# Kernel tuning notes

Hardware: AMD Instinct MI355X
Metric: run time of the kernel (lower is better)

## Reference

```python
import jax, jax.numpy as jnp
import numpy as np

NUM_EXPERTS = 16
CAPACITY = 1024  # expert_capacity


def setup_inputs() -> dict:
    key = jax.random.key(0)
    ks = jax.random.split(key, 5)
    B, D, H, O = 8192, 1024, 4096, 1024
    E = NUM_EXPERTS
    sc = lambda k, shp, fan: jax.random.normal(k, shp, jnp.float32) * (1.0 / np.sqrt(fan))
    return {
        "x": jax.random.normal(ks[0], (B, D), jnp.float32),
        "Wr": sc(ks[1], (D, E), D),
        "br": jnp.zeros((E,), jnp.float32),
        "W1": sc(ks[2], (E, D, H), D),
        "b1": jnp.zeros((E, H), jnp.float32),
        "W2": sc(ks[3], (E, H, O), H),
        "b2": jnp.zeros((E, O), jnp.float32),
    }


def reference(x, Wr, br, W1, b1, W2, b2):
    B = x.shape[0]
    E = Wr.shape[1]
    O = W2.shape[-1]
    cap = min(CAPACITY, B)

    router_logits = x @ Wr + br                 # [B, E]
    # NOTE: softmax over the TOKEN axis (dim=0), as in the source (expert-choice)
    router_probs = jax.nn.softmax(router_logits, axis=0)

    # each expert picks its top-`cap` tokens
    top_scores, top_idx = jax.lax.top_k(router_probs.T, cap)   # [E, cap]

    sel = x[top_idx]                            # [E, cap, D] gather
    h = jax.nn.relu(jnp.einsum('ecd,edh->ech', sel, W1) + b1[:, None, :])
    # dropout_prob=0 -> identity in eval/our config
    eo = jnp.einsum('ech,eho->eco', h, W2) + b2[:, None, :]    # [E, cap, O]

    contrib = eo * top_scores[..., None]        # weight by routing score
    output = jnp.zeros((B, O), x.dtype).at[top_idx.reshape(-1)].add(
        contrib.reshape(-1, O))                 # scatter-add combine

    expert_mask = jnp.zeros((B, E), x.dtype).at[
        top_idx, jnp.arange(E)[:, None]].set(1.0)
    return output, router_probs, expert_mask
```

## Files before the change

### kernel.cpp

```cpp
#include <hip/hip_runtime.h>

typedef unsigned short u16;
typedef unsigned int   u32;
typedef unsigned long long u64;
typedef __attribute__((ext_vector_type(8))) short s16x8;
typedef __attribute__((ext_vector_type(4))) float f32x4;

constexpr int B = 8192, D = 1024, H = 4096, O = 1024, E = 16, CAP = 1024;
constexpr int EG = 4;
constexpr int NGROUP = E / EG;

__device__ __forceinline__ u16 f2bf(float f) {
  u32 u = __float_as_uint(f);
  u32 r = (u + 0x7FFFu + ((u >> 16) & 1u)) >> 16;
  return (u16)r;
}

__global__ __launch_bounds__(256) void zero_kernel(float4* __restrict__ p, int n4) {
  int i = blockIdx.x * blockDim.x + threadIdx.x;
  int stride = gridDim.x * blockDim.x;
  float4 z; z.x = z.y = z.z = z.w = 0.0f;
  for (; i < n4; i += stride) p[i] = z;
}

__global__ __launch_bounds__(256) void router_kernel(const float* __restrict__ x,
    const float* __restrict__ Wr, const float* __restrict__ br,
    float* __restrict__ logits) {
  int t = blockIdx.x * 256 + threadIdx.x;
  int b = t >> 4, e = t & 15;
  const float* xr = x + (size_t)b * D;
  float acc = 0.f;
#pragma unroll 8
  for (int k = 0; k < D; k++) acc = fmaf(xr[k], Wr[k * E + e], acc);
  logits[t] = acc + br[e];
}

__global__ __launch_bounds__(1024) void softmax_colwise(const float* __restrict__ logits,
                                                        float* __restrict__ probs) {
  __shared__ float red[16];
  int e = blockIdx.x, t = threadIdx.x;
  float l[8];
  float mx = -1e30f;
#pragma unroll
  for (int i = 0; i < 8; i++) {
    l[i] = logits[(size_t)(t + i * 1024) * E + e];
    mx = fmaxf(mx, l[i]);
  }
#pragma unroll
  for (int o = 32; o > 0; o >>= 1) mx = fmaxf(mx, __shfl_xor(mx, o));
  if ((t & 63) == 0) red[t >> 6] = mx;
  __syncthreads();
  if (t < 64) {
    float v = (t < 16) ? red[t] : -1e30f;
#pragma unroll
    for (int o = 8; o > 0; o >>= 1) v = fmaxf(v, __shfl_xor(v, o));
    if (t == 0) red[0] = v;
  }
  __syncthreads();
  mx = red[0];
  __syncthreads();
  float s = 0.f;
#pragma unroll
  for (int i = 0; i < 8; i++) { l[i] = expf(l[i] - mx); s += l[i]; }
#pragma unroll
  for (int o = 32; o > 0; o >>= 1) s += __shfl_xor(s, o);
  if ((t & 63) == 0) red[t >> 6] = s;
  __syncthreads();
  if (t < 64) {
    float v = (t < 16) ? red[t] : 0.f;
#pragma unroll
    for (int o = 8; o > 0; o >>= 1) v += __shfl_xor(v, o);
    if (t == 0) red[0] = v;
  }
  __syncthreads();
  float inv = 1.0f / red[0];
#pragma unroll
  for (int i = 0; i < 8; i++)
    probs[(size_t)(t + i * 1024) * E + e] = l[i] * inv;
}

__global__ __launch_bounds__(1024) void topk_bitonic(const float* __restrict__ probs,
    float* __restrict__ scores, int* __restrict__ tidx, float* __restrict__ mask) {
  __shared__ u64 d[8192];
  int e = blockIdx.x, t = threadIdx.x;
  for (int i = t; i < B; i += 1024) {
    float p = probs[(size_t)i * E + e];
    d[i] = ((u64)__float_as_uint(p) << 32) | (u32)(0xFFFFFFFFu - (u32)i);
  }
  __syncthreads();
  for (int k = 2; k <= B; k <<= 1) {
    for (int j = k >> 1; j > 0; j >>= 1) {
      for (int i = t; i < B; i += 1024) {
        int l = i ^ j;
        if (l > i) {
          u64 a = d[i], b2 = d[l];
          bool descBlk = (i & k) == 0;
          if (descBlk ? (a < b2) : (a > b2)) { d[i] = b2; d[l] = a; }
        }
      }
      __syncthreads();
    }
  }
  u64 v = d[t];
  float p = __uint_as_float((u32)(v >> 32));
  int b = (int)(0xFFFFFFFFu - (u32)v);
  scores[e * CAP + t] = p;
  tidx[e * CAP + t] = b;
  mask[(size_t)b * E + e] = 1.0f;
}

__global__ __launch_bounds__(256) void gather_bf16(const float* __restrict__ x,
    const int* __restrict__ tidx, u16* __restrict__ Abf) {
  int blk = blockIdx.x;
  int row = tidx[blk];
  const float4* src = (const float4*)(x + (size_t)row * D);
  int t = threadIdx.x;
  float4 v = src[t];
  uint2 u;
  u.x = f2bf(v.x) | ((u32)f2bf(v.y) << 16);
  u.y = f2bf(v.z) | ((u32)f2bf(v.w) << 16);
  ((uint2*)(Abf + (size_t)blk * D))[t] = u;
}

template <int DR, int DC>
__global__ __launch_bounds__(256) void transpose_convert(const float* __restrict__ in,
                                                         u16* __restrict__ out) {
  __shared__ float tile[64][68];
  constexpr int TR = DR / 64, TC = DC / 64;
  int bid = blockIdx.x;
  int e = bid / (TR * TC);
  int rem = bid % (TR * TC);
  int tr = rem / TC, tc = rem % TC;
  int t = threadIdx.x;
  int r0 = t >> 4;
  int c0 = (t & 15) << 2;
  const float* src = in + (size_t)e * DR * DC + (size_t)(tr * 64) * DC + (size_t)tc * 64;
#pragma unroll
  for (int p = 0; p < 4; p++) {
    float4 v = *(const float4*)(src + (size_t)(p * 16 + r0) * DC + c0);
    tile[p * 16 + r0][c0 + 0] = v.x;
    tile[p * 16 + r0][c0 + 1] = v.y;
    tile[p * 16 + r0][c0 + 2] = v.z;
    tile[p * 16 + r0][c0 + 3] = v.w;
  }
  __syncthreads();
  u16* dst = out + (size_t)e * DR * DC + (size_t)(tc * 64) * DR + (size_t)tr * 64;
#pragma unroll
  for (int p = 0; p < 4; p++) {
    int hl = p * 16 + r0;
    uint2 u;
    u.x = f2bf(tile[c0 + 0][hl]) | ((u32)f2bf(tile[c0 + 1][hl]) << 16);
    u.y = f2bf(tile[c0 + 2][hl]) | ((u32)f2bf(tile[c0 + 3][hl]) << 16);
    *(uint2*)(dst + (size_t)hl * DR + c0) = u;
  }
}

template <int EPI, int NTOT, int KTOT>
__global__ __launch_bounds__(256, 2) void moe_gemm(const u16* __restrict__ A,
    const u16* __restrict__ Bt, const float* __restrict__ bias,
    u16* __restrict__ Hout, float* __restrict__ outp,
    const float* __restrict__ scores, const int* __restrict__ tidx) {
  constexpr int NTM = 1024 / 128, NTN = NTOT / 128, NKT = KTOT / 64;
  __shared__ u16 Alds[128 * 64];
  __shared__ u16 Blds[128 * 64];
  int bid = blockIdx.x;
  int e = bid / (NTM * NTN);
  int rem = bid % (NTM * NTN);
  int tm = rem / NTN, tn = rem % NTN;
  int tid = threadIdx.x, w = tid >> 6, lane = tid & 63;
  int wr = w >> 1, wc = w & 1;

  const u16* Abase = A + ((size_t)e * 1024 + tm * 128) * KTOT;
  const u16* Bbase = Bt + ((size_t)e * NTOT + tn * 128) * KTOT;
  int srow = lane >> 3;
  int scol = (lane & 7) * 8;

  f32x4 acc[4][4];
#pragma unroll
  for (int m = 0; m < 4; m++)
#pragma unroll
    for (int n = 0; n < 4; n++) { f32x4 z = {0.f, 0.f, 0.f, 0.f}; acc[m][n] = z; }

  for (int kt = 0; kt < NKT; kt++) {
    const u16* Ak = Abase + kt * 64;
    const u16* Bk = Bbase + kt * 64;
#pragma unroll
    for (int i = 0; i < 4; i++) {
      int grp = w * 4 + i;
      int row = grp * 8 + srow;
      __builtin_amdgcn_global_load_lds(
          (const __attribute__((address_space(1))) void*)(Ak + (size_t)row * KTOT + scol),
          (__attribute__((address_space(3))) void*)(&Alds[grp * 512]), 16, 0, 0);
      __builtin_amdgcn_global_load_lds(
          (const __attribute__((address_space(1))) void*)(Bk + (size_t)row * KTOT + scol),
          (__attribute__((address_space(3))) void*)(&Blds[grp * 512]), 16, 0, 0);
    }
    __syncthreads();
#pragma unroll
    for (int kk = 0; kk < 2; kk++) {
      int kb = kk * 32 + (lane >> 4) * 8;
      s16x8 a[4], bfr[4];
#pragma unroll
      for (int m = 0; m < 4; m++)
        a[m] = *(const s16x8*)&Alds[(wr * 64 + m * 16 + (lane & 15)) * 64 + kb];
#pragma unroll
      for (int n = 0; n < 4; n++)
        bfr[n] = *(const s16x8*)&Blds[(wc * 64 + n * 16 + (lane & 15)) * 64 + kb];
#pragma unroll
      for (int m = 0; m < 4; m++)
#pragma unroll
        for (int n = 0; n < 4; n++)
          acc[m][n] = __builtin_amdgcn_mfma_f32_16x16x32_bf16(a[m], bfr[n], acc[m][n], 0, 0, 0);
    }
    __syncthreads();
  }

  int colb = tn * 128 + wc * 64 + (lane & 15);
  float bv[4];
#pragma unroll
  for (int n = 0; n < 4; n++) bv[n] = bias[(size_t)e * NTOT + colb + n * 16];

  if constexpr (EPI == 0) {
    u16* Hb = Hout + (size_t)e * 1024 * NTOT;
#pragma unroll
    for (int m = 0; m < 4; m++) {
#pragma unroll
      for (int j = 0; j < 4; j++) {
        int r = tm * 128 + wr * 64 + m * 16 + (lane >> 4) * 4 + j;
#pragma unroll
        for (int n = 0; n < 4; n++) {
          float v = acc[m][n][j] + bv[n];
          v = fmaxf(v, 0.0f);
          Hb[(size_t)r * NTOT + colb + n * 16] = f2bf(v);
        }
      }
    }
  } else {
#pragma unroll
    for (int m = 0; m < 4; m++) {
#pragma unroll
      for (int j = 0; j < 4; j++) {
        int rc = tm * 128 + wr * 64 + m * 16 + (lane >> 4) * 4 + j;
        float sc = scores[e * CAP + rc];
        int tok = tidx[e * CAP + rc];
        float* orow = outp + (size_t)tok * O;
#pragma unroll
        for (int n = 0; n < 4; n++) {
          float v = (acc[m][n][j] + bv[n]) * sc;
          atomicAdd(&orow[colb + n * 16], v);
        }
      }
    }
  }
}

extern "C" void kernel_launch(void* const* d_in, const int* in_sizes, int n_in,
                              void* d_out, int out_size, void* d_ws, size_t ws_size,
                              hipStream_t stream) {
  const float* x  = (const float*)d_in[0];
  const float* Wr = (const float*)d_in[1];
  const float* br = (const float*)d_in[2];
  const float* W1 = (const float*)d_in[3];
  const float* b1 = (const float*)d_in[4];
  const float* W2 = (const float*)d_in[5];
  const float* b2 = (const float*)d_in[6];

  float* out   = (float*)d_out;
  float* probs = out + (size_t)B * O;
  float* mask  = probs + (size_t)B * E;

  char* ws = (char*)d_ws;
  float* logits  = (float*)ws;
  float* scoresW = (float*)(ws + (512u << 10));
  int*   idxW    = (int*)(ws + (576u << 10));
  u16* Abf = (u16*)(ws + (1u << 20));
  u16* Wt  = (u16*)(ws + (1u << 20) + (32u << 20));
  u16* Hbf = (u16*)(ws + (1u << 20) + (64u << 20));
  if (ws_size < ((1u << 20) + (96u << 20))) return;

  zero_kernel<<<2048, 256, 0, stream>>>((float4*)d_out, (B * O + 2 * B * E) / 4);
  router_kernel<<<(B * E) / 256, 256, 0, stream>>>(x, Wr, br, logits);
  softmax_colwise<<<E, 1024, 0, stream>>>(logits, probs);
  topk_bitonic<<<E, 1024, 0, stream>>>(probs, scoresW, idxW, mask);
  gather_bf16<<<E * CAP, 256, 0, stream>>>(x, idxW, Abf);

  for (int g = 0; g < NGROUP; g++) {
    const float* W1g = W1 + (size_t)g * EG * D * H;
    const float* W2g = W2 + (size_t)g * EG * H * O;
    transpose_convert<D, H><<<EG * (D / 64) * (H / 64), 256, 0, stream>>>(W1g, Wt);
    moe_gemm<0, H, D><<<EG * 8 * (H / 128), 256, 0, stream>>>(
        Abf + (size_t)g * EG * CAP * D, Wt, b1 + (size_t)g * EG * H,
        Hbf, nullptr, nullptr, nullptr);
    transpose_convert<H, O><<<EG * (H / 64) * (O / 64), 256, 0, stream>>>(W2g, Wt);
    moe_gemm<1, O, H><<<EG * 8 * (O / 128), 256, 0, stream>>>(
        Hbf, Wt, b2 + (size_t)g * EG * O,
        nullptr, out, scoresW + (size_t)g * EG * CAP, idxW + (size_t)g * EG * CAP);
  }
}
```

Baseline: 1.327 ms.

## Radix-select top-k, ungroup expert GEMMs, vectorize router, remap GEMM block order

Replaces the bitonic sort top-k with an 8-bit radix select over 64-bit keys, then compacts the selected tokens via an atomic counter. Drops the 4-expert grouping so all weights are transposed and each GEMM runs in a single launch over all experts, using separate W1t/W2t buffers in a larger workspace. Adds a block-index swizzle in the GEMM, float4 loads in the router, and stops zeroing the probs region. The cost is more workspace memory, and the selected tokens are no longer written in sorted order.

```diff
diff --git a/kernel.cpp b/kernel.cpp
--- a/kernel.cpp
+++ b/kernel.cpp
@@ -7,8 +7,6 @@
 typedef __attribute__((ext_vector_type(4))) float f32x4;
 
 constexpr int B = 8192, D = 1024, H = 4096, O = 1024, E = 16, CAP = 1024;
-constexpr int EG = 4;
-constexpr int NGROUP = E / EG;
 
 __device__ __forceinline__ u16 f2bf(float f) {
   u32 u = __float_as_uint(f);
@@ -16,11 +14,13 @@
   return (u16)r;
 }
 
-__global__ __launch_bounds__(256) void zero_kernel(float4* __restrict__ p, int n4) {
+__global__ __launch_bounds__(256) void zero_kernel(float4* __restrict__ outp, int n4o,
+                                                   float4* __restrict__ maskp, int n4m) {
   int i = blockIdx.x * blockDim.x + threadIdx.x;
   int stride = gridDim.x * blockDim.x;
   float4 z; z.x = z.y = z.z = z.w = 0.0f;
-  for (; i < n4; i += stride) p[i] = z;
+  for (int j = i; j < n4o; j += stride) outp[j] = z;
+  for (int j = i; j < n4m; j += stride) maskp[j] = z;
 }
 
 __global__ __launch_bounds__(256) void router_kernel(const float* __restrict__ x,
@@ -28,10 +28,17 @@
     float* __restrict__ logits) {
   int t = blockIdx.x * 256 + threadIdx.x;
   int b = t >> 4, e = t & 15;
-  const float* xr = x + (size_t)b * D;
+  const float4* xr = (const float4*)(x + (size_t)b * D);
   float acc = 0.f;
-#pragma unroll 8
-  for (int k = 0; k < D; k++) acc = fmaf(xr[k], Wr[k * E + e], acc);
+#pragma unroll 4
+  for (int k = 0; k < D / 4; k++) {
+    float4 v = xr[k];
+    const float* wc = Wr + (size_t)(k * 4) * E + e;
+    acc = fmaf(v.x, wc[0], acc);
+    acc = fmaf(v.y, wc[E], acc);
+    acc = fmaf(v.z, wc[2 * E], acc);
+    acc = fmaf(v.w, wc[3 * E], acc);
+  }
   logits[t] = acc + br[e];
 }
 
@@ -79,34 +86,55 @@
     probs[(size_t)(t + i * 1024) * E + e] = l[i] * inv;
 }
 
-__global__ __launch_bounds__(1024) void topk_bitonic(const float* __restrict__ probs,
+__global__ __launch_bounds__(1024) void topk_radix(const float* __restrict__ probs,
     float* __restrict__ scores, int* __restrict__ tidx, float* __restrict__ mask) {
-  __shared__ u64 d[8192];
+  __shared__ u64 keys[8192];
+  __shared__ u32 hist[256];
+  __shared__ u64 pref_s;
+  __shared__ u32 k_s;
+  __shared__ u32 cnt_s;
   int e = blockIdx.x, t = threadIdx.x;
   for (int i = t; i < B; i += 1024) {
     float p = probs[(size_t)i * E + e];
-    d[i] = ((u64)__float_as_uint(p) << 32) | (u32)(0xFFFFFFFFu - (u32)i);
-  }
-  __syncthreads();
-  for (int k = 2; k <= B; k <<= 1) {
-    for (int j = k >> 1; j > 0; j >>= 1) {
-      for (int i = t; i < B; i += 1024) {
-        int l = i ^ j;
-        if (l > i) {
-          u64 a = d[i], b2 = d[l];
-          bool descBlk = (i & k) == 0;
-          if (descBlk ? (a < b2) : (a > b2)) { d[i] = b2; d[l] = a; }
-        }
+    keys[i] = ((u64)__float_as_uint(p) << 32) | (u32)(0xFFFFFFFFu - (u32)i);
+  }
+  if (t == 0) cnt_s = 0;
+  __syncthreads();
+  u64 prefix = 0; u32 k = CAP;
+  for (int shift = 56; shift >= 0; shift -= 8) {
+    if (t < 256) hist[t] = 0;
+    __syncthreads();
+    u64 himask = (shift == 56) ? 0ull : (~0ull << (shift + 8));
+    for (int i = t; i < B; i += 1024) {
+      u64 kk = keys[i];
+      if ((kk & himask) == (prefix & himask))
+        atomicAdd(&hist[(u32)(kk >> shift) & 255u], 1u);
+    }
+    __syncthreads();
+    if (t == 0) {
+      u32 acc = 0; int bb = 255;
+      for (; bb >= 0; bb--) {
+        if (acc + hist[bb] >= k) break;
+        acc += hist[bb];
       }
-      __syncthreads();
-    }
-  }
-  u64 v = d[t];
-  float p = __uint_as_float((u32)(v >> 32));
-  int b = (int)(0xFFFFFFFFu - (u32)v);
-  scores[e * CAP + t] = p;
-  tidx[e * CAP + t] = b;
-  mask[(size_t)b * E + e] = 1.0f;
+      if (bb < 0) bb = 0;
+      pref_s = prefix | ((u64)(u32)bb << shift);
+      k_s = k - acc;
+    }
+    __syncthreads();
+    prefix = pref_s; k = k_s;
+    __syncthreads();
+  }
+  for (int i = t; i < B; i += 1024) {
+    u64 kk = keys[i];
+    if (kk >= prefix) {
+      u32 slot = atomicAdd(&cnt_s, 1u);
+      scores[e * CAP + slot] = __uint_as_float((u32)(kk >> 32));
+      int b = (int)(0xFFFFFFFFu - (u32)kk);
+      tidx[e * CAP + slot] = b;
+      mask[(size_t)b * E + e] = 1.0f;
+    }
+  }
 }
 
 __global__ __launch_bounds__(256) void gather_bf16(const float* __restrict__ x,
@@ -161,9 +189,11 @@
     u16* __restrict__ Hout, float* __restrict__ outp,
     const float* __restrict__ scores, const int* __restrict__ tidx) {
   constexpr int NTM = 1024 / 128, NTN = NTOT / 128, NKT = KTOT / 64;
+  constexpr int NWG = E * NTM * NTN;
   __shared__ u16 Alds[128 * 64];
   __shared__ u16 Blds[128 * 64];
   int bid = blockIdx.x;
+  bid = (bid & 7) * (NWG / 8) + (bid >> 3);
   int e = bid / (NTM * NTN);
   int rem = bid % (NTM * NTN);
   int tm = rem / NTN, tn = rem % NTN;
@@ -273,27 +303,23 @@
   float* logits  = (float*)ws;
   float* scoresW = (float*)(ws + (512u << 10));
   int*   idxW    = (int*)(ws + (576u << 10));
-  u16* Abf = (u16*)(ws + (1u << 20));
-  u16* Wt  = (u16*)(ws + (1u << 20) + (32u << 20));
-  u16* Hbf = (u16*)(ws + (1u << 20) + (64u << 20));
-  if (ws_size < ((1u << 20) + (96u << 20))) return;
-
-  zero_kernel<<<2048, 256, 0, stream>>>((float4*)d_out, (B * O + 2 * B * E) / 4);
+  u16* Abf = (u16*)(ws + (1u   << 20));
+  u16* W1t = (u16*)(ws + (33u  << 20));
+  u16* W2t = (u16*)(ws + (161u << 20));
+  u16* Hbf = (u16*)(ws + (289u << 20));
+  if (ws_size < (417u << 20)) return;
+
+  zero_kernel<<<2048, 256, 0, stream>>>((float4*)out, (B * O) / 4,
+                                        (float4*)mask, (B * E) / 4);
   router_kernel<<<(B * E) / 256, 256, 0, stream>>>(x, Wr, br, logits);
   softmax_colwise<<<E, 1024, 0, stream>>>(logits, probs);
-  topk_bitonic<<<E, 1024, 0, stream>>>(probs, scoresW, idxW, mask);
+  topk_radix<<<E, 1024, 0, stream>>>(probs, scoresW, idxW, mask);
   gather_bf16<<<E * CAP, 256, 0, stream>>>(x, idxW, Abf);
 
-  for (int g = 0; g < NGROUP; g++) {
-    const float* W1g = W1 + (size_t)g * EG * D * H;
-    const float* W2g = W2 + (size_t)g * EG * H * O;
-    transpose_convert<D, H><<<EG * (D / 64) * (H / 64), 256, 0, stream>>>(W1g, Wt);
-    moe_gemm<0, H, D><<<EG * 8 * (H / 128), 256, 0, stream>>>(
-        Abf + (size_t)g * EG * CAP * D, Wt, b1 + (size_t)g * EG * H,
-        Hbf, nullptr, nullptr, nullptr);
-    transpose_convert<H, O><<<EG * (H / 64) * (O / 64), 256, 0, stream>>>(W2g, Wt);
-    moe_gemm<1, O, H><<<EG * 8 * (O / 128), 256, 0, stream>>>(
-        Hbf, Wt, b2 + (size_t)g * EG * O,
-        nullptr, out, scoresW + (size_t)g * EG * CAP, idxW + (size_t)g * EG * CAP);
-  }
-}
+  transpose_convert<D, H><<<E * (D / 64) * (H / 64), 256, 0, stream>>>(W1, W1t);
+  moe_gemm<0, H, D><<<E * 8 * (H / 128), 256, 0, stream>>>(
+      Abf, W1t, b1, Hbf, nullptr, nullptr, nullptr);
+  transpose_convert<H, O><<<E * (H / 64) * (O / 64), 256, 0, stream>>>(W2, W2t);
+  moe_gemm<1, O, H><<<E * 8 * (O / 128), 256, 0, stream>>>(
+      Hbf, W2t, b2, nullptr, out, scoresW, idxW);
+}
```

Result: faster. 1.062 ms (-19.9%).
